# Optimization experiments

Hardware: AMD Instinct MI355X
Metric: run time of the kernel (lower is better)

## Reference

```python
import jax, jax.numpy as jnp
import numpy as np

B, T_DEC, F = 16, 32, 8
S_ENC, H, L = 256, 512, 2
TGT_IDX = jnp.arange(8)  # target_indices = all features


def setup_inputs() -> dict:
    key = jax.random.key(0)
    ks = jax.random.split(key, 16)
    g = lambda k, shp, s=0.05: jax.random.normal(k, shp, dtype=jnp.float32) * s
    return {
        'target': jax.random.normal(ks[0], (B, T_DEC, F), dtype=jnp.float32),
        'hidden0': jax.random.normal(ks[1], (L, B, H), dtype=jnp.float32),
        'enc_outputs': jax.random.normal(ks[2], (B, S_ENC, H), dtype=jnp.float32),
        # Attention params
        'attn_W': g(ks[3], (H, 2 * H)), 'attn_b': jnp.zeros((H,), jnp.float32),
        'v_w': g(ks[4], (H,)),
        # GRU layer 0 (input = F + H) and layer 1 (input = H); PyTorch layout [3H, in]
        'gru_Wih0': g(ks[5], (3 * H, F + H)), 'gru_Whh0': g(ks[6], (3 * H, H)),
        'gru_bih0': jnp.zeros((3 * H,), jnp.float32), 'gru_bhh0': jnp.zeros((3 * H,), jnp.float32),
        'gru_Wih1': g(ks[7], (3 * H, H)), 'gru_Whh1': g(ks[8], (3 * H, H)),
        'gru_bih1': jnp.zeros((3 * H,), jnp.float32), 'gru_bhh1': jnp.zeros((3 * H,), jnp.float32),
        # output Linear (2H + F -> F)
        'out_W': g(ks[9], (F, 2 * H + F)), 'out_b': jnp.zeros((F,), jnp.float32),
        'input_seq_len': S_ENC,
    }


def _gru_cell(x, h, Wih, Whh, bih, bhh):
    # PyTorch GRUCell math; gate order [r, z, n]
    gi = x @ Wih.T + bih
    gh = h @ Whh.T + bhh
    ir, iz, inn = jnp.split(gi, 3, axis=-1)
    hr, hz, hn = jnp.split(gh, 3, axis=-1)
    r = jax.nn.sigmoid(ir + hr)
    z = jax.nn.sigmoid(iz + hz)
    n = jnp.tanh(inn + r * hn)
    return (1.0 - z) * n + z * h


def reference(target, hidden0, enc_outputs, attn_W, attn_b, v_w,
              gru_Wih0, gru_Whh0, gru_bih0, gru_bhh0,
              gru_Wih1, gru_Whh1, gru_bih1, gru_bhh1,
              out_W, out_b, input_seq_len):
    b, s, h = enc_outputs.shape

    def step(carry, target_t):
        hidden, x_in = carry  # hidden [L,B,H], x_in [B,F]
        h_top = hidden[-1]
        # Bahdanau attention
        hid_rep = jnp.broadcast_to(h_top[:, None, :], (b, s, h))
        energy = jnp.tanh(jnp.concatenate([hid_rep, enc_outputs], axis=-1) @ attn_W.T + attn_b)
        scores = energy @ v_w  # [B,S]
        weightings = jax.nn.softmax(scores, axis=1)
        weighted = jnp.einsum('bs,bsh->bh', weightings, enc_outputs)  # [B,H]
        # stacked GRU single step
        x = jnp.concatenate([x_in, weighted], axis=-1)  # [B, F+H]
        h0 = _gru_cell(x, hidden[0], gru_Wih0, gru_Whh0, gru_bih0, gru_bhh0)
        h1 = _gru_cell(h0, hidden[1], gru_Wih1, gru_Whh1, gru_bih1, gru_bhh1)
        new_hidden = jnp.stack([h0, h1])
        # output projection + relu (applied in DecoderBase.forward)
        out = jnp.concatenate([h1, weighted, x_in], axis=-1) @ out_W.T + out_b
        out = jax.nn.relu(out)  # [B,F]
        # no teacher forcing (teacher_force_prob=None): replace target features with prediction
        next_in = target_t.at[:, TGT_IDX].set(out)
        return (new_hidden, next_in), out

    target_ts = jnp.swapaxes(target, 0, 1)  # [T,B,F]
    (_, _), outs = jax.lax.scan(step, (hidden0, target[:, 0, :]), target_ts)
    return jnp.swapaxes(outs, 0, 1)  # [B,T,F]
```

## Files before the change

kernel.cpp:

```cpp
#include <hip/hip_runtime.h>


namespace {
constexpr int NTHR_P = 256, NBLK_P = 256;
constexpr int NTHR = 256, NBLK = 256;

constexpr int OFF_FLG     = 0;
constexpr int OFF_HIDP_LL = 4096;
constexpr int OFF_H0LL    = 20480;
constexpr int OFF_H1LL    = 28672;
constexpr int OFF_ATTP    = 36864;
constexpr int OFF_AEH     = 168448;
constexpr int OFF_WHID    = OFF_AEH + 131072;
constexpr int OFF_WIH0    = OFF_WHID + 131072;
constexpr int OFF_WHH0    = OFF_WIH0 + 399360;
constexpr int OFF_WIH1    = OFF_WHH0 + 393216;
constexpr int OFF_WHH1    = OFF_WIH1 + 393216;
constexpr int OFF_ENCP    = OFF_WHH1 + 393216;

constexpr int L_H1   = 0;
constexpr int L_H0   = 256;
constexpr int L_HIDP = 512;
constexpr int L_ES   = 1024;
constexpr int L_HX   = 1040;
constexpr int L_AX   = 1304;
constexpr int L_AH   = 1400;
constexpr int L_HS   = 1496;
constexpr int L_BIH0 = 1528, L_BHH0 = 1624, L_BIH1 = 1720, L_BHH1 = 1816;
constexpr int L_VW   = 1912;
constexpr int L_XIN  = 2424;
constexpr int LDS_FLOATS = 2432;
}

typedef _Float16 h2 __attribute__((ext_vector_type(2)));
union U32H { unsigned u; h2 h; };

__device__ __forceinline__ float dot2(unsigned a, unsigned b, float acc) {
    U32H ua, ub; ua.u = a; ub.u = b;
#if __has_builtin(__builtin_amdgcn_fdot2)
    return __builtin_amdgcn_fdot2(ua.h, ub.h, acc, false);
#else
    return acc + (float)ua.h.x * (float)ub.h.x + (float)ua.h.y * (float)ub.h.y;
#endif
}
__device__ __forceinline__ unsigned packh2(float a, float b) {
    U32H u; u.h = h2{(_Float16)a, (_Float16)b}; return u.u;
}
__device__ __forceinline__ float fsig(float x) { return 1.0f / (1.0f + __expf(-x)); }
__device__ __forceinline__ float ftanhf(float x) {
    float e = __expf(2.0f * x);
    return 1.0f - 2.0f / (e + 1.0f);
}
__device__ __forceinline__ float cload(const float* p) {
    return __hip_atomic_load(p, __ATOMIC_RELAXED, __HIP_MEMORY_SCOPE_SYSTEM);
}
__device__ __forceinline__ void cstore(float* p, float v) {
    __hip_atomic_store(p, v, __ATOMIC_RELAXED, __HIP_MEMORY_SCOPE_SYSTEM);
}
__device__ __forceinline__ unsigned ucload(const unsigned* p) {
    return __hip_atomic_load(p, __ATOMIC_RELAXED, __HIP_MEMORY_SCOPE_SYSTEM);
}

__device__ __forceinline__ void ll_store(unsigned long long* p, unsigned payload,
                                         unsigned stamp) {
    unsigned long long v = (unsigned long long)payload | ((unsigned long long)stamp << 32);
    asm volatile("global_store_dwordx2 %0, %1, off sc0 sc1" :: "v"(p), "v"(v) : "memory");
}
__device__ __forceinline__ unsigned long long ll_load(const unsigned long long* p) {
    unsigned long long v;
    asm volatile("global_load_dwordx2 %0, %1, off sc0 sc1\n\ts_waitcnt vmcnt(0)"
                 : "=v"(v) : "v"(p) : "memory");
    return v;
}
__device__ __forceinline__ unsigned ll_poll(const unsigned long long* p, unsigned stamp) {
    for (;;) {
        unsigned long long v = ll_load(p);
        if ((unsigned)(v >> 32) == stamp) return (unsigned)v;
        __builtin_amdgcn_s_sleep(1);
    }
}
__device__ __forceinline__ void flag_store(unsigned* p, unsigned v) {
    asm volatile("global_store_dword %0, %1, off sc0 sc1" :: "v"(p), "v"(v) : "memory");
}

__global__ __launch_bounds__(NTHR_P) void pack_kernel(
    const float* __restrict__ attn_W, const float* __restrict__ Wih0,
    const float* __restrict__ Whh0, const float* __restrict__ Wih1,
    const float* __restrict__ Whh1, float* __restrict__ ws) {
    unsigned* aehU  = (unsigned*)(ws + OFF_AEH);
    unsigned* whidU = (unsigned*)(ws + OFF_WHID);
    unsigned* wih0U = (unsigned*)(ws + OFF_WIH0);
    unsigned* whh0U = (unsigned*)(ws + OFF_WHH0);
    unsigned* wih1U = (unsigned*)(ws + OFF_WIH1);
    unsigned* whh1U = (unsigned*)(ws + OFF_WHH1);
    const int gtid = blockIdx.x * NTHR_P + threadIdx.x;
    for (int i = gtid; i < 131072; i += NBLK_P * NTHR_P) {
        const int jr = i >> 8, p = i & 255;
        aehU[i]  = packh2(attn_W[jr * 1024 + 512 + 2 * p], attn_W[jr * 1024 + 513 + 2 * p]);
        whidU[i] = packh2(attn_W[jr * 1024 + 2 * p], attn_W[jr * 1024 + 1 + 2 * p]);
    }
    for (int i = gtid; i < 399360; i += NBLK_P * NTHR_P)
        wih0U[i] = packh2(Wih0[2 * i], Wih0[2 * i + 1]);
    for (int i = gtid; i < 393216; i += NBLK_P * NTHR_P) {
        whh0U[i] = packh2(Whh0[2 * i], Whh0[2 * i + 1]);
        wih1U[i] = packh2(Wih1[2 * i], Wih1[2 * i + 1]);
        whh1U[i] = packh2(Whh1[2 * i], Whh1[2 * i + 1]);
    }
}

__global__ __launch_bounds__(NTHR_P) void encp_kernel(
    const float* __restrict__ enc, const float* __restrict__ attn_b,
    float* __restrict__ ws) {
    const int tid = threadIdx.x, bid = blockIdx.x;
    const int b = bid >> 4, s = bid & 15;
    const unsigned* aehU = (const unsigned*)(ws + OFF_AEH);
    unsigned* encpU = (unsigned*)(ws + OFF_ENCP);
    __shared__ __align__(16) float lds[8192];
    for (int i = 0; i < 32; ++i) {
        const int idx = tid + i * 256;
        lds[idx] = enc[(b * 256 + s * 16) * 512 + idx];
    }
    __syncthreads();
    float a0[16], a1[16];
    const float bb0 = attn_b[2 * tid], bb1 = attn_b[2 * tid + 1];
#pragma unroll
    for (int sl = 0; sl < 16; ++sl) { a0[sl] = bb0; a1[sl] = bb1; }
    const unsigned* w0 = &aehU[(2 * tid) * 256];
    const unsigned* w1 = &aehU[(2 * tid + 1) * 256];
    for (int p = 0; p < 256; ++p) {
        const unsigned ww0 = w0[p], ww1 = w1[p];
#pragma unroll
        for (int sl = 0; sl < 16; ++sl) {
            const unsigned epk = packh2(lds[sl * 512 + 2 * p], lds[sl * 512 + 2 * p + 1]);
            a0[sl] = dot2(epk, ww0, a0[sl]);
            a1[sl] = dot2(epk, ww1, a1[sl]);
        }
    }
    for (int sl = 0; sl < 16; ++sl)
        encpU[(b * 256 + s * 16 + sl) * 256 + tid] = packh2(a0[sl], a1[sl]);
}

__global__ __launch_bounds__(NTHR) void decoder_kernel(
    const float* __restrict__ target, const float* __restrict__ hidden0,
    const float* __restrict__ enc, const float* __restrict__ v_w,
    const float* __restrict__ bih0, const float* __restrict__ bhh0,
    const float* __restrict__ bih1, const float* __restrict__ bhh1,
    const float* __restrict__ outW, const float* __restrict__ outBias,
    float* __restrict__ out, float* __restrict__ ws) {
    const int tid = threadIdx.x, bid = blockIdx.x;
    const int b = bid >> 4, s = bid & 15;

    unsigned* flg = (unsigned*)ws + OFF_FLG;
    unsigned long long* hidpLL = (unsigned long long*)(ws + OFF_HIDP_LL);
    unsigned long long* h0LL = (unsigned long long*)(ws + OFF_H0LL);
    unsigned long long* h1LL = (unsigned long long*)(ws + OFF_H1LL);
    float* attP = ws + OFF_ATTP;
    const unsigned* whidU = (const unsigned*)(ws + OFF_WHID);
    const unsigned* wih0U = (const unsigned*)(ws + OFF_WIH0);
    const unsigned* whh0U = (const unsigned*)(ws + OFF_WHH0);
    const unsigned* wih1U = (const unsigned*)(ws + OFF_WIH1);
    const unsigned* whh1U = (const unsigned*)(ws + OFF_WHH1);
    const unsigned* encpU = (const unsigned*)(ws + OFF_ENCP);

    __shared__ __align__(16) float lds[LDS_FLOATS];
    unsigned* ldsU = (unsigned*)lds;

    if (tid < 96) {
        const int grow = (tid >> 5) * 512 + s * 32 + (tid & 31);
        lds[L_BIH0 + tid] = bih0[grow]; lds[L_BHH0 + tid] = bhh0[grow];
        lds[L_BIH1 + tid] = bih1[grow]; lds[L_BHH1 + tid] = bhh1[grow];
    }
    lds[L_VW + tid] = v_w[tid];
    lds[L_VW + 256 + tid] = v_w[256 + tid];
    ldsU[L_H0 + tid] = packh2(hidden0[b * 512 + 2 * tid], hidden0[b * 512 + 2 * tid + 1]);
    ldsU[L_H1 + tid] = packh2(hidden0[8192 + b * 512 + 2 * tid],
                              hidden0[8192 + b * 512 + 2 * tid + 1]);
    if (tid < 8) lds[L_XIN + tid] = target[b * 256 + tid];
    if (tid < 4) ldsU[L_HX + 260 + tid] = 0u;
    __syncthreads();

    for (int t = 0; t < 32; ++t) {
        const unsigned tgt = (unsigned)(t + 1);

        {
            const int r = tid >> 3, sub = tid & 7;
            const uint4* wrow = (const uint4*)&whidU[(s * 32 + r) * 256 + sub * 32];
            const uint4* h1p = (const uint4*)&ldsU[L_H1 + sub * 32];
            float acc = 0.f;
#pragma unroll
            for (int k4 = 0; k4 < 8; ++k4) {
                const uint4 hv = h1p[k4], wv = wrow[k4];
                acc = dot2(hv.x, wv.x, acc); acc = dot2(hv.y, wv.y, acc);
                acc = dot2(hv.z, wv.z, acc); acc = dot2(hv.w, wv.w, acc);
            }
            acc += __shfl_down(acc, 4, 8); acc += __shfl_down(acc, 2, 8); acc += __shfl_down(acc, 1, 8);
            if (sub == 0) ll_store(&hidpLL[b * 512 + s * 32 + r], __float_as_uint(acc), tgt);
        }
        lds[L_HIDP + tid] = __uint_as_float(ll_poll(&hidpLL[b * 512 + tid], tgt));
        lds[L_HIDP + 256 + tid] = __uint_as_float(ll_poll(&hidpLL[b * 512 + 256 + tid], tgt));
        __syncthreads();

        {
            const int sloc = tid >> 4, sub = tid & 15;
            const unsigned* ep = &encpU[(b * 256 + s * 16 + sloc) * 256];
            float acc = 0.f;
#pragma unroll 4
            for (int k2 = 0; k2 < 16; ++k2) {
                const int p = k2 * 16 + sub;
                U32H u; u.u = ep[p];
                acc += lds[L_VW + 2 * p] * ftanhf((float)u.h.x + lds[L_HIDP + 2 * p]);
                acc += lds[L_VW + 2 * p + 1] * ftanhf((float)u.h.y + lds[L_HIDP + 2 * p + 1]);
            }
            acc += __shfl_down(acc, 8, 16); acc += __shfl_down(acc, 4, 16);
            acc += __shfl_down(acc, 2, 16); acc += __shfl_down(acc, 1, 16);
            if (sub == 0) lds[L_ES + sloc] = __expf(acc);
        }
        __syncthreads();
        {
            float wp0 = 0.f, wp1 = 0.f;
            const float2* er = (const float2*)&enc[(b * 256 + s * 16) * 512];
#pragma unroll
            for (int sl = 0; sl < 16; ++sl) {
                const float2 e = er[sl * 256 + tid];
                const float es = lds[L_ES + sl];
                wp0 += es * e.x; wp1 += es * e.y;
            }
            cstore(&attP[(b * 16 + s) * 514 + 2 * tid], wp0);
            cstore(&attP[(b * 16 + s) * 514 + 2 * tid + 1], wp1);
            if (tid == 0) {
                float l = 0.f;
#pragma unroll
                for (int i = 0; i < 16; ++i) l += lds[L_ES + i];
                cstore(&attP[(b * 16 + s) * 514 + 512], l);
            }
        }
        asm volatile("s_waitcnt vmcnt(0)" ::: "memory");
        if ((tid & 63) == 0)
            flag_store(&flg[(b * 16 + s) * 16 + (tid >> 6) * 4], tgt);

        if (tid < 64) {
            const unsigned* fp = &flg[(b * 16 + (tid >> 2)) * 16 + (tid & 3) * 4];
            while (ucload(fp) < tgt) __builtin_amdgcn_s_sleep(1);
        }
        __syncthreads();
        __builtin_amdgcn_fence(__ATOMIC_ACQUIRE, "workgroup");
        {
            float w0 = 0.f, w1 = 0.f;
            for (int sp = 0; sp < 16; ++sp) {
                w0 += cload(&attP[(b * 16 + sp) * 514 + 2 * tid]);
                w1 += cload(&attP[(b * 16 + sp) * 514 + 2 * tid + 1]);
            }
            if (tid < 16) lds[L_ES + tid] = cload(&attP[(b * 16 + tid) * 514 + 512]);
            __syncthreads();
            float L = 0.f;
#pragma unroll
            for (int i = 0; i < 16; ++i) L += lds[L_ES + i];
            const float inv = 1.f / L;
            ldsU[L_HX + 4 + tid] = packh2(w0 * inv, w1 * inv);
            if (tid < 4) {
                ldsU[L_HX + tid] = packh2(lds[L_XIN + 2 * tid], lds[L_XIN + 2 * tid + 1]);
            }
        }
        __syncthreads();

        if (tid < 192) {
            const int u = tid >> 1, sub = tid & 1;
            const int gh = u >> 5, r = u & 31;
            const int grow = gh * 512 + s * 32 + r;
            const uint4* wx = (const uint4*)&wih0U[grow * 260 + sub * 132];
            const uint4* xp = (const uint4*)&ldsU[L_HX + sub * 132];
            float ax = 0.f;
#pragma unroll 11
            for (int k4 = 0; k4 < 33; ++k4) {
                const uint4 xv = xp[k4], wv = wx[k4];
                ax = dot2(xv.x, wv.x, ax); ax = dot2(xv.y, wv.y, ax);
                ax = dot2(xv.z, wv.z, ax); ax = dot2(xv.w, wv.w, ax);
            }
            const uint4* wh = (const uint4*)&whh0U[grow * 256 + sub * 128];
            const uint4* hp = (const uint4*)&ldsU[L_H0 + sub * 128];
            float ah = 0.f;
#pragma unroll 8
            for (int k4 = 0; k4 < 32; ++k4) {
                const uint4 hv = hp[k4], wv = wh[k4];
                ah = dot2(hv.x, wv.x, ah); ah = dot2(hv.y, wv.y, ah);
                ah = dot2(hv.z, wv.z, ah); ah = dot2(hv.w, wv.w, ah);
            }
            ax += __shfl_down(ax, 1, 2); ah += __shfl_down(ah, 1, 2);
            if (sub == 0) {
                lds[L_AX + u] = ax + lds[L_BIH0 + u];
                lds[L_AH + u] = ah + lds[L_BHH0 + u];
            }
        }
        __syncthreads();
        if (tid < 32) {
            const int r = tid;
            const float rg = fsig(lds[L_AX + r] + lds[L_AH + r]);
            const float z = fsig(lds[L_AX + 32 + r] + lds[L_AH + 32 + r]);
            const float n = ftanhf(lds[L_AX + 64 + r] + rg * lds[L_AH + 64 + r]);
            U32H u; u.u = ldsU[L_H0 + s * 16 + (r >> 1)];
            const float hold = (r & 1) ? (float)u.h.y : (float)u.h.x;
            lds[L_HS + r] = (1.f - z) * n + z * hold;
        }
        __syncthreads();
        if (tid < 16)
            ll_store(&h0LL[(b * 16 + s) * 16 + tid],
                     packh2(lds[L_HS + 2 * tid], lds[L_HS + 2 * tid + 1]), tgt);
        {
            const int sp = tid >> 4, jj = tid & 15;
            ldsU[L_H0 + sp * 16 + jj] = ll_poll(&h0LL[(b * 16 + sp) * 16 + jj], tgt);
        }
        __syncthreads();

        if (tid < 192) {
            const int u = tid >> 1, sub = tid & 1;
            const int gh = u >> 5, r = u & 31;
            const int grow = gh * 512 + s * 32 + r;
            const uint4* wx = (const uint4*)&wih1U[grow * 256 + sub * 128];
            const uint4* xp = (const uint4*)&ldsU[L_H0 + sub * 128];
            float ax = 0.f;
#pragma unroll 8
            for (int k4 = 0; k4 < 32; ++k4) {
                const uint4 xv = xp[k4], wv = wx[k4];
                ax = dot2(xv.x, wv.x, ax); ax = dot2(xv.y, wv.y, ax);
                ax = dot2(xv.z, wv.z, ax); ax = dot2(xv.w, wv.w, ax);
            }
            const uint4* wh = (const uint4*)&whh1U[grow * 256 + sub * 128];
            const uint4* hp = (const uint4*)&ldsU[L_H1 + sub * 128];
            float ah = 0.f;
#pragma unroll 8
            for (int k4 = 0; k4 < 32; ++k4) {
                const uint4 hv = hp[k4], wv = wh[k4];
                ah = dot2(hv.x, wv.x, ah); ah = dot2(hv.y, wv.y, ah);
                ah = dot2(hv.z, wv.z, ah); ah = dot2(hv.w, wv.w, ah);
            }
            ax += __shfl_down(ax, 1, 2); ah += __shfl_down(ah, 1, 2);
            if (sub == 0) {
                lds[L_AX + u] = ax + lds[L_BIH1 + u];
                lds[L_AH + u] = ah + lds[L_BHH1 + u];
            }
        }
        __syncthreads();
        if (tid < 32) {
            const int r = tid;
            const float rg = fsig(lds[L_AX + r] + lds[L_AH + r]);
            const float z = fsig(lds[L_AX + 32 + r] + lds[L_AH + 32 + r]);
            const float n = ftanhf(lds[L_AX + 64 + r] + rg * lds[L_AH + 64 + r]);
            U32H u; u.u = ldsU[L_H1 + s * 16 + (r >> 1)];
            const float hold = (r & 1) ? (float)u.h.y : (float)u.h.x;
            lds[L_HS + r] = (1.f - z) * n + z * hold;
        }
        __syncthreads();
        if (tid < 16)
            ll_store(&h1LL[(b * 16 + s) * 16 + tid],
                     packh2(lds[L_HS + 2 * tid], lds[L_HS + 2 * tid + 1]), tgt);
        {
            const int sp = tid >> 4, jj = tid & 15;
            ldsU[L_H1 + sp * 16 + jj] = ll_poll(&h1LL[(b * 16 + sp) * 16 + jj], tgt);
        }
        __syncthreads();

        {
            const int f = tid >> 5, l = tid & 31;
            const float* ow = &outW[f * 1032];
            float acc = 0.f;
#pragma unroll
            for (int i = 0; i < 8; ++i) {
                const int k2 = i * 32 + l;
                U32H u; u.u = ldsU[L_H1 + k2];
                acc += ow[2 * k2] * (float)u.h.x + ow[2 * k2 + 1] * (float)u.h.y;
            }
#pragma unroll
            for (int i = 0; i < 8; ++i) {
                const int k2 = i * 32 + l;
                U32H u; u.u = ldsU[L_HX + 4 + k2];
                acc += ow[512 + 2 * k2] * (float)u.h.x + ow[512 + 2 * k2 + 1] * (float)u.h.y;
            }
            if (l < 8) acc += ow[1024 + l] * lds[L_XIN + l];
            acc += __shfl_down(acc, 16, 32); acc += __shfl_down(acc, 8, 32);
            acc += __shfl_down(acc, 4, 32); acc += __shfl_down(acc, 2, 32);
            acc += __shfl_down(acc, 1, 32);
            if (l == 0) {
                const float o = fmaxf(acc + outBias[f], 0.f);
                lds[L_ES + f] = o;
                if (s == 0) out[b * 256 + t * 8 + f] = o;
            }
        }
        __syncthreads();
        if (tid < 8) lds[L_XIN + tid] = lds[L_ES + tid];
        __syncthreads();
    }
}

extern "C" void kernel_launch(void* const* d_in, const int* in_sizes, int n_in,
                              void* d_out, int out_size, void* d_ws, size_t ws_size,
                              hipStream_t stream) {
    (void)in_sizes; (void)n_in; (void)out_size; (void)ws_size;
    hipMemsetAsync(d_ws, 0, 147456, stream);
    pack_kernel<<<NBLK_P, NTHR_P, 0, stream>>>(
        (const float*)d_in[3], (const float*)d_in[6], (const float*)d_in[7],
        (const float*)d_in[10], (const float*)d_in[11], (float*)d_ws);
    encp_kernel<<<NBLK_P, NTHR_P, 0, stream>>>(
        (const float*)d_in[2], (const float*)d_in[4], (float*)d_ws);
    decoder_kernel<<<NBLK, NTHR, 0, stream>>>(
        (const float*)d_in[0], (const float*)d_in[1], (const float*)d_in[2],
        (const float*)d_in[5], (const float*)d_in[8], (const float*)d_in[9],
        (const float*)d_in[12], (const float*)d_in[13], (const float*)d_in[14],
        (const float*)d_in[15], (float*)d_out, (float*)d_ws);
}
```

Measured before the change: 1.040 ms.

## Fuse pack and encoder-projection into persistent decoder, overlap recurrent matvecs with polls

Merges the weight-packing and encoder-projection kernels into the persistent decoder kernel, separated by a software grid barrier, which removes two kernel launches. Each block now computes the full hidden-attention projection redundantly instead of exchanging partial results through global flags, dropping one cross-block exchange per step. The Whh matvecs and the output-projection partial sums are moved ahead of the cross-block polls so they overlap with waiting. The cost is redundant per-block work and reliance on all 256 blocks being co-resident for the grid barrier.

```diff
diff --git a/kernel.cpp b/kernel.cpp
--- a/kernel.cpp
+++ b/kernel.cpp
@@ -2,11 +2,9 @@
 
 
 namespace {
-constexpr int NTHR_P = 256, NBLK_P = 256;
 constexpr int NTHR = 256, NBLK = 256;
 
 constexpr int OFF_FLG     = 0;
-constexpr int OFF_HIDP_LL = 4096;
 constexpr int OFF_H0LL    = 20480;
 constexpr int OFF_H1LL    = 28672;
 constexpr int OFF_ATTP    = 36864;
@@ -22,14 +20,16 @@
 constexpr int L_H0   = 256;
 constexpr int L_HIDP = 512;
 constexpr int L_ES   = 1024;
-constexpr int L_HX   = 1040;
-constexpr int L_AX   = 1304;
-constexpr int L_AH   = 1400;
-constexpr int L_HS   = 1496;
-constexpr int L_BIH0 = 1528, L_BHH0 = 1624, L_BIH1 = 1720, L_BHH1 = 1816;
-constexpr int L_VW   = 1912;
-constexpr int L_XIN  = 2424;
-constexpr int LDS_FLOATS = 2432;
+constexpr int L_HX   = 1280;
+constexpr int L_AX   = 1544;
+constexpr int L_AH   = 1640;
+constexpr int L_AH1  = 1736;
+constexpr int L_HS   = 1832;
+constexpr int L_OWP  = 1864;
+constexpr int L_BIH0 = 1872, L_BHH0 = 1968, L_BIH1 = 2064, L_BHH1 = 2160;
+constexpr int L_VW   = 2256;
+constexpr int L_XIN  = 2768;
+constexpr int LDS_FLOATS = 8192;
 }
 
 typedef _Float16 h2 __attribute__((ext_vector_type(2)));
@@ -83,87 +83,87 @@
     asm volatile("global_store_dword %0, %1, off sc0 sc1" :: "v"(p), "v"(v) : "memory");
 }
 
-__global__ __launch_bounds__(NTHR_P) void pack_kernel(
-    const float* __restrict__ attn_W, const float* __restrict__ Wih0,
-    const float* __restrict__ Whh0, const float* __restrict__ Wih1,
-    const float* __restrict__ Whh1, float* __restrict__ ws) {
+__device__ __forceinline__ void bar_sync_flush(unsigned* cnt, unsigned target) {
+    __syncthreads();
+    if (threadIdx.x == 0) {
+        __builtin_amdgcn_fence(__ATOMIC_RELEASE, "agent");
+        __hip_atomic_fetch_add(cnt, 1u, __ATOMIC_RELAXED, __HIP_MEMORY_SCOPE_SYSTEM);
+        while (__hip_atomic_load(cnt, __ATOMIC_RELAXED, __HIP_MEMORY_SCOPE_SYSTEM) < target)
+            __builtin_amdgcn_s_sleep(8);
+        __builtin_amdgcn_fence(__ATOMIC_ACQUIRE, "agent");
+    }
+    __syncthreads();
+}
+
+__global__ __launch_bounds__(NTHR) void decoder_kernel(
+    const float* __restrict__ target, const float* __restrict__ hidden0,
+    const float* __restrict__ enc, const float* __restrict__ attn_W,
+    const float* __restrict__ attn_b, const float* __restrict__ v_w,
+    const float* __restrict__ Wih0, const float* __restrict__ Whh0,
+    const float* __restrict__ bih0, const float* __restrict__ bhh0,
+    const float* __restrict__ Wih1, const float* __restrict__ Whh1,
+    const float* __restrict__ bih1, const float* __restrict__ bhh1,
+    const float* __restrict__ outW, const float* __restrict__ outBias,
+    float* __restrict__ out, float* __restrict__ ws) {
+    const int tid = threadIdx.x, bid = blockIdx.x;
+    const int b = bid >> 4, s = bid & 15;
+
+    unsigned* flg = (unsigned*)ws + OFF_FLG;
+    unsigned* gridCnt = (unsigned*)ws + 8192;
+    unsigned long long* h0LL = (unsigned long long*)(ws + OFF_H0LL);
+    unsigned long long* h1LL = (unsigned long long*)(ws + OFF_H1LL);
+    float* attP = ws + OFF_ATTP;
     unsigned* aehU  = (unsigned*)(ws + OFF_AEH);
     unsigned* whidU = (unsigned*)(ws + OFF_WHID);
     unsigned* wih0U = (unsigned*)(ws + OFF_WIH0);
     unsigned* whh0U = (unsigned*)(ws + OFF_WHH0);
     unsigned* wih1U = (unsigned*)(ws + OFF_WIH1);
     unsigned* whh1U = (unsigned*)(ws + OFF_WHH1);
-    const int gtid = blockIdx.x * NTHR_P + threadIdx.x;
-    for (int i = gtid; i < 131072; i += NBLK_P * NTHR_P) {
+    unsigned* encpU = (unsigned*)(ws + OFF_ENCP);
+
+    __shared__ __align__(16) float lds[LDS_FLOATS];
+    unsigned* ldsU = (unsigned*)lds;
+    const int gtid = bid * NTHR + tid;
+
+    for (int i = gtid; i < 131072; i += NBLK * NTHR) {
         const int jr = i >> 8, p = i & 255;
         aehU[i]  = packh2(attn_W[jr * 1024 + 512 + 2 * p], attn_W[jr * 1024 + 513 + 2 * p]);
         whidU[i] = packh2(attn_W[jr * 1024 + 2 * p], attn_W[jr * 1024 + 1 + 2 * p]);
     }
-    for (int i = gtid; i < 399360; i += NBLK_P * NTHR_P)
+    for (int i = gtid; i < 399360; i += NBLK * NTHR)
         wih0U[i] = packh2(Wih0[2 * i], Wih0[2 * i + 1]);
-    for (int i = gtid; i < 393216; i += NBLK_P * NTHR_P) {
+    for (int i = gtid; i < 393216; i += NBLK * NTHR) {
         whh0U[i] = packh2(Whh0[2 * i], Whh0[2 * i + 1]);
         wih1U[i] = packh2(Wih1[2 * i], Wih1[2 * i + 1]);
         whh1U[i] = packh2(Whh1[2 * i], Whh1[2 * i + 1]);
     }
-}
-
-__global__ __launch_bounds__(NTHR_P) void encp_kernel(
-    const float* __restrict__ enc, const float* __restrict__ attn_b,
-    float* __restrict__ ws) {
-    const int tid = threadIdx.x, bid = blockIdx.x;
-    const int b = bid >> 4, s = bid & 15;
-    const unsigned* aehU = (const unsigned*)(ws + OFF_AEH);
-    unsigned* encpU = (unsigned*)(ws + OFF_ENCP);
-    __shared__ __align__(16) float lds[8192];
-    for (int i = 0; i < 32; ++i) {
-        const int idx = tid + i * 256;
-        lds[idx] = enc[(b * 256 + s * 16) * 512 + idx];
-    }
-    __syncthreads();
-    float a0[16], a1[16];
-    const float bb0 = attn_b[2 * tid], bb1 = attn_b[2 * tid + 1];
-#pragma unroll
-    for (int sl = 0; sl < 16; ++sl) { a0[sl] = bb0; a1[sl] = bb1; }
-    const unsigned* w0 = &aehU[(2 * tid) * 256];
-    const unsigned* w1 = &aehU[(2 * tid + 1) * 256];
-    for (int p = 0; p < 256; ++p) {
-        const unsigned ww0 = w0[p], ww1 = w1[p];
-#pragma unroll
-        for (int sl = 0; sl < 16; ++sl) {
-            const unsigned epk = packh2(lds[sl * 512 + 2 * p], lds[sl * 512 + 2 * p + 1]);
-            a0[sl] = dot2(epk, ww0, a0[sl]);
-            a1[sl] = dot2(epk, ww1, a1[sl]);
-        }
-    }
-    for (int sl = 0; sl < 16; ++sl)
-        encpU[(b * 256 + s * 16 + sl) * 256 + tid] = packh2(a0[sl], a1[sl]);
-}
-
-__global__ __launch_bounds__(NTHR) void decoder_kernel(
-    const float* __restrict__ target, const float* __restrict__ hidden0,
-    const float* __restrict__ enc, const float* __restrict__ v_w,
-    const float* __restrict__ bih0, const float* __restrict__ bhh0,
-    const float* __restrict__ bih1, const float* __restrict__ bhh1,
-    const float* __restrict__ outW, const float* __restrict__ outBias,
-    float* __restrict__ out, float* __restrict__ ws) {
-    const int tid = threadIdx.x, bid = blockIdx.x;
-    const int b = bid >> 4, s = bid & 15;
-
-    unsigned* flg = (unsigned*)ws + OFF_FLG;
-    unsigned long long* hidpLL = (unsigned long long*)(ws + OFF_HIDP_LL);
-    unsigned long long* h0LL = (unsigned long long*)(ws + OFF_H0LL);
-    unsigned long long* h1LL = (unsigned long long*)(ws + OFF_H1LL);
-    float* attP = ws + OFF_ATTP;
-    const unsigned* whidU = (const unsigned*)(ws + OFF_WHID);
-    const unsigned* wih0U = (const unsigned*)(ws + OFF_WIH0);
-    const unsigned* whh0U = (const unsigned*)(ws + OFF_WHH0);
-    const unsigned* wih1U = (const unsigned*)(ws + OFF_WIH1);
-    const unsigned* whh1U = (const unsigned*)(ws + OFF_WHH1);
-    const unsigned* encpU = (const unsigned*)(ws + OFF_ENCP);
-
-    __shared__ __align__(16) float lds[LDS_FLOATS];
-    unsigned* ldsU = (unsigned*)lds;
+    bar_sync_flush(gridCnt, NBLK);
+
+    {
+        for (int i = 0; i < 32; ++i) {
+            const int idx = tid + i * 256;
+            lds[idx] = enc[(b * 256 + s * 16) * 512 + idx];
+        }
+        __syncthreads();
+        float a0[16], a1[16];
+        const float bb0 = attn_b[2 * tid], bb1 = attn_b[2 * tid + 1];
+#pragma unroll
+        for (int sl = 0; sl < 16; ++sl) { a0[sl] = bb0; a1[sl] = bb1; }
+        const unsigned* w0 = &aehU[(2 * tid) * 256];
+        const unsigned* w1 = &aehU[(2 * tid + 1) * 256];
+        for (int p = 0; p < 256; ++p) {
+            const unsigned ww0 = w0[p], ww1 = w1[p];
+#pragma unroll
+            for (int sl = 0; sl < 16; ++sl) {
+                const unsigned epk = packh2(lds[sl * 512 + 2 * p], lds[sl * 512 + 2 * p + 1]);
+                a0[sl] = dot2(epk, ww0, a0[sl]);
+                a1[sl] = dot2(epk, ww1, a1[sl]);
+            }
+        }
+        for (int sl = 0; sl < 16; ++sl)
+            encpU[(b * 256 + s * 16 + sl) * 256 + tid] = packh2(a0[sl], a1[sl]);
+        __syncthreads();
+    }
 
     if (tid < 96) {
         const int grow = (tid >> 5) * 512 + s * 32 + (tid & 31);
@@ -183,21 +183,24 @@
         const unsigned tgt = (unsigned)(t + 1);
 
         {
-            const int r = tid >> 3, sub = tid & 7;
-            const uint4* wrow = (const uint4*)&whidU[(s * 32 + r) * 256 + sub * 32];
-            const uint4* h1p = (const uint4*)&ldsU[L_H1 + sub * 32];
-            float acc = 0.f;
-#pragma unroll
-            for (int k4 = 0; k4 < 8; ++k4) {
-                const uint4 hv = h1p[k4], wv = wrow[k4];
-                acc = dot2(hv.x, wv.x, acc); acc = dot2(hv.y, wv.y, acc);
-                acc = dot2(hv.z, wv.z, acc); acc = dot2(hv.w, wv.w, acc);
-            }
-            acc += __shfl_down(acc, 4, 8); acc += __shfl_down(acc, 2, 8); acc += __shfl_down(acc, 1, 8);
-            if (sub == 0) ll_store(&hidpLL[b * 512 + s * 32 + r], __float_as_uint(acc), tgt);
-        }
-        lds[L_HIDP + tid] = __uint_as_float(ll_poll(&hidpLL[b * 512 + tid], tgt));
-        lds[L_HIDP + 256 + tid] = __uint_as_float(ll_poll(&hidpLL[b * 512 + 256 + tid], tgt));
+            const uint4* h1v = (const uint4*)&ldsU[L_H1];
+#pragma unroll
+            for (int half = 0; half < 2; ++half) {
+                const int row = half * 256 + tid;
+                const uint4* w = (const uint4*)&whidU[row * 256];
+                float a0 = 0.f, a1 = 0.f;
+#pragma unroll 8
+                for (int k = 0; k < 64; k += 2) {
+                    const uint4 wv0 = w[k], hv0 = h1v[k];
+                    a0 = dot2(hv0.x, wv0.x, a0); a0 = dot2(hv0.y, wv0.y, a0);
+                    a0 = dot2(hv0.z, wv0.z, a0); a0 = dot2(hv0.w, wv0.w, a0);
+                    const uint4 wv1 = w[k + 1], hv1 = h1v[k + 1];
+                    a1 = dot2(hv1.x, wv1.x, a1); a1 = dot2(hv1.y, wv1.y, a1);
+                    a1 = dot2(hv1.z, wv1.z, a1); a1 = dot2(hv1.w, wv1.w, a1);
+                }
+                lds[L_HIDP + row] = a0 + a1;
+            }
+        }
         __syncthreads();
 
         {
@@ -238,6 +241,23 @@
         if ((tid & 63) == 0)
             flag_store(&flg[(b * 16 + s) * 16 + (tid >> 6) * 4], tgt);
 
+        if (tid < 192) {
+            const int u = tid >> 1, sub = tid & 1;
+            const int gh = u >> 5, r = u & 31;
+            const int grow = gh * 512 + s * 32 + r;
+            const uint4* wh = (const uint4*)&whh0U[grow * 256 + sub * 128];
+            const uint4* hp = (const uint4*)&ldsU[L_H0 + sub * 128];
+            float ah = 0.f;
+#pragma unroll 8
+            for (int k4 = 0; k4 < 32; ++k4) {
+                const uint4 hv = hp[k4], wv = wh[k4];
+                ah = dot2(hv.x, wv.x, ah); ah = dot2(hv.y, wv.y, ah);
+                ah = dot2(hv.z, wv.z, ah); ah = dot2(hv.w, wv.w, ah);
+            }
+            ah += __shfl_down(ah, 1, 2);
+            if (sub == 0) lds[L_AH + u] = ah + lds[L_BHH0 + u];
+        }
+
         if (tid < 64) {
             const unsigned* fp = &flg[(b * 16 + (tid >> 2)) * 16 + (tid & 3) * 4];
             while (ucload(fp) < tgt) __builtin_amdgcn_s_sleep(1);
@@ -257,9 +277,8 @@
             for (int i = 0; i < 16; ++i) L += lds[L_ES + i];
             const float inv = 1.f / L;
             ldsU[L_HX + 4 + tid] = packh2(w0 * inv, w1 * inv);
-            if (tid < 4) {
+            if (tid < 4)
                 ldsU[L_HX + tid] = packh2(lds[L_XIN + 2 * tid], lds[L_XIN + 2 * tid + 1]);
-            }
         }
         __syncthreads();
 
@@ -276,20 +295,8 @@
                 ax = dot2(xv.x, wv.x, ax); ax = dot2(xv.y, wv.y, ax);
                 ax = dot2(xv.z, wv.z, ax); ax = dot2(xv.w, wv.w, ax);
             }
-            const uint4* wh = (const uint4*)&whh0U[grow * 256 + sub * 128];
-            const uint4* hp = (const uint4*)&ldsU[L_H0 + sub * 128];
-            float ah = 0.f;
-#pragma unroll 8
-            for (int k4 = 0; k4 < 32; ++k4) {
-                const uint4 hv = hp[k4], wv = wh[k4];
-                ah = dot2(hv.x, wv.x, ah); ah = dot2(hv.y, wv.y, ah);
-                ah = dot2(hv.z, wv.z, ah); ah = dot2(hv.w, wv.w, ah);
-            }
-            ax += __shfl_down(ax, 1, 2); ah += __shfl_down(ah, 1, 2);
-            if (sub == 0) {
-                lds[L_AX + u] = ax + lds[L_BIH0 + u];
-                lds[L_AH + u] = ah + lds[L_BHH0 + u];
-            }
+            ax += __shfl_down(ax, 1, 2);
+            if (sub == 0) lds[L_AX + u] = ax + lds[L_BIH0 + u];
         }
         __syncthreads();
         if (tid < 32) {
@@ -303,11 +310,32 @@
         }
         __syncthreads();
         if (tid < 16)
-            ll_store(&h0LL[(b * 16 + s) * 16 + tid],
+            ll_store(&h0LL[b * 256 + s * 16 + tid],
                      packh2(lds[L_HS + 2 * tid], lds[L_HS + 2 * tid + 1]), tgt);
-        {
-            const int sp = tid >> 4, jj = tid & 15;
-            ldsU[L_H0 + sp * 16 + jj] = ll_poll(&h0LL[(b * 16 + sp) * 16 + jj], tgt);
+
+        if (tid < 192) {
+            const int u = tid >> 1, sub = tid & 1;
+            const int gh = u >> 5, r = u & 31;
+            const int grow = gh * 512 + s * 32 + r;
+            const uint4* wh = (const uint4*)&whh1U[grow * 256 + sub * 128];
+            const uint4* hp = (const uint4*)&ldsU[L_H1 + sub * 128];
+            float ah = 0.f;
+#pragma unroll 8
+            for (int k4 = 0; k4 < 32; ++k4) {
+                const uint4 hv = hp[k4], wv = wh[k4];
+                ah = dot2(hv.x, wv.x, ah); ah = dot2(hv.y, wv.y, ah);
+                ah = dot2(hv.z, wv.z, ah); ah = dot2(hv.w, wv.w, ah);
+            }
+            ah += __shfl_down(ah, 1, 2);
+            if (sub == 0) lds[L_AH1 + u] = ah + lds[L_BHH1 + u];
+        }
+
+        if (tid < 64) {
+#pragma unroll
+            for (int i = 0; i < 4; ++i) {
+                const int idx = tid * 4 + i;
+                ldsU[L_H0 + idx] = ll_poll(&h0LL[b * 256 + idx], tgt);
+            }
         }
         __syncthreads();
 
@@ -324,38 +352,47 @@
                 ax = dot2(xv.x, wv.x, ax); ax = dot2(xv.y, wv.y, ax);
                 ax = dot2(xv.z, wv.z, ax); ax = dot2(xv.w, wv.w, ax);
             }
-            const uint4* wh = (const uint4*)&whh1U[grow * 256 + sub * 128];
-            const uint4* hp = (const uint4*)&ldsU[L_H1 + sub * 128];
-            float ah = 0.f;
-#pragma unroll 8
-            for (int k4 = 0; k4 < 32; ++k4) {
-                const uint4 hv = hp[k4], wv = wh[k4];
-                ah = dot2(hv.x, wv.x, ah); ah = dot2(hv.y, wv.y, ah);
-                ah = dot2(hv.z, wv.z, ah); ah = dot2(hv.w, wv.w, ah);
-            }
-            ax += __shfl_down(ax, 1, 2); ah += __shfl_down(ah, 1, 2);
-            if (sub == 0) {
-                lds[L_AX + u] = ax + lds[L_BIH1 + u];
-                lds[L_AH + u] = ah + lds[L_BHH1 + u];
-            }
+            ax += __shfl_down(ax, 1, 2);
+            if (sub == 0) lds[L_AX + u] = ax + lds[L_BIH1 + u];
         }
         __syncthreads();
         if (tid < 32) {
             const int r = tid;
-            const float rg = fsig(lds[L_AX + r] + lds[L_AH + r]);
-            const float z = fsig(lds[L_AX + 32 + r] + lds[L_AH + 32 + r]);
-            const float n = ftanhf(lds[L_AX + 64 + r] + rg * lds[L_AH + 64 + r]);
+            const float rg = fsig(lds[L_AX + r] + lds[L_AH1 + r]);
+            const float z = fsig(lds[L_AX + 32 + r] + lds[L_AH1 + 32 + r]);
+            const float n = ftanhf(lds[L_AX + 64 + r] + rg * lds[L_AH1 + 64 + r]);
             U32H u; u.u = ldsU[L_H1 + s * 16 + (r >> 1)];
             const float hold = (r & 1) ? (float)u.h.y : (float)u.h.x;
             lds[L_HS + r] = (1.f - z) * n + z * hold;
         }
         __syncthreads();
         if (tid < 16)
-            ll_store(&h1LL[(b * 16 + s) * 16 + tid],
+            ll_store(&h1LL[b * 256 + s * 16 + tid],
                      packh2(lds[L_HS + 2 * tid], lds[L_HS + 2 * tid + 1]), tgt);
-        {
-            const int sp = tid >> 4, jj = tid & 15;
-            ldsU[L_H1 + sp * 16 + jj] = ll_poll(&h1LL[(b * 16 + sp) * 16 + jj], tgt);
+
+        {
+            const int f = tid >> 5, l = tid & 31;
+            const float* ow = &outW[f * 1032 + 512];
+            float acc = 0.f;
+#pragma unroll
+            for (int i = 0; i < 8; ++i) {
+                const int k2 = i * 32 + l;
+                U32H u; u.u = ldsU[L_HX + 4 + k2];
+                acc += ow[2 * k2] * (float)u.h.x + ow[2 * k2 + 1] * (float)u.h.y;
+            }
+            if (l < 8) acc += outW[f * 1032 + 1024 + l] * lds[L_XIN + l];
+            acc += __shfl_down(acc, 16, 32); acc += __shfl_down(acc, 8, 32);
+            acc += __shfl_down(acc, 4, 32); acc += __shfl_down(acc, 2, 32);
+            acc += __shfl_down(acc, 1, 32);
+            if (l == 0) lds[L_OWP + f] = acc;
+        }
+
+        if (tid < 64) {
+#pragma unroll
+            for (int i = 0; i < 4; ++i) {
+                const int idx = tid * 4 + i;
+                ldsU[L_H1 + idx] = ll_poll(&h1LL[b * 256 + idx], tgt);
+            }
         }
         __syncthreads();
 
@@ -369,18 +406,11 @@
                 U32H u; u.u = ldsU[L_H1 + k2];
                 acc += ow[2 * k2] * (float)u.h.x + ow[2 * k2 + 1] * (float)u.h.y;
             }
-#pragma unroll
-            for (int i = 0; i < 8; ++i) {
-                const int k2 = i * 32 + l;
-                U32H u; u.u = ldsU[L_HX + 4 + k2];
-                acc += ow[512 + 2 * k2] * (float)u.h.x + ow[512 + 2 * k2 + 1] * (float)u.h.y;
-            }
-            if (l < 8) acc += ow[1024 + l] * lds[L_XIN + l];
             acc += __shfl_down(acc, 16, 32); acc += __shfl_down(acc, 8, 32);
             acc += __shfl_down(acc, 4, 32); acc += __shfl_down(acc, 2, 32);
             acc += __shfl_down(acc, 1, 32);
             if (l == 0) {
-                const float o = fmaxf(acc + outBias[f], 0.f);
+                const float o = fmaxf(acc + lds[L_OWP + f] + outBias[f], 0.f);
                 lds[L_ES + f] = o;
                 if (s == 0) out[b * 256 + t * 8 + f] = o;
             }
@@ -396,14 +426,11 @@
                               hipStream_t stream) {
     (void)in_sizes; (void)n_in; (void)out_size; (void)ws_size;
     hipMemsetAsync(d_ws, 0, 147456, stream);
-    pack_kernel<<<NBLK_P, NTHR_P, 0, stream>>>(
-        (const float*)d_in[3], (const float*)d_in[6], (const float*)d_in[7],
-        (const float*)d_in[10], (const float*)d_in[11], (float*)d_ws);
-    encp_kernel<<<NBLK_P, NTHR_P, 0, stream>>>(
-        (const float*)d_in[2], (const float*)d_in[4], (float*)d_ws);
     decoder_kernel<<<NBLK, NTHR, 0, stream>>>(
         (const float*)d_in[0], (const float*)d_in[1], (const float*)d_in[2],
-        (const float*)d_in[5], (const float*)d_in[8], (const float*)d_in[9],
+        (const float*)d_in[3], (const float*)d_in[4], (const float*)d_in[5],
+        (const float*)d_in[6], (const float*)d_in[7], (const float*)d_in[8],
+        (const float*)d_in[9], (const float*)d_in[10], (const float*)d_in[11],
         (const float*)d_in[12], (const float*)d_in[13], (const float*)d_in[14],
         (const float*)d_in[15], (float*)d_out, (float*)d_ws);
 }
```

Measured after the change: 1.471 ms. 1.41x slower.
